# Optimization experiments

Hardware: AMD Instinct MI355X
Metric: run time of the kernel (lower is better)

Reference implementation:

```python
import jax, jax.numpy as jnp
import numpy as np

N = 50000      # nodes
E = 800000     # edges (avg degree 16)
IN = 128; HID = 128; OUT = 128; HEADS = 4
NEG_SLOPE = 0.2


def setup_inputs() -> dict:
    key = jax.random.key(0)
    ks = jax.random.split(key, 16)
    def glorot(k, shape):
        fan = shape[0] if len(shape) == 2 else int(np.prod(shape))
        return jax.random.normal(k, shape, jnp.float32) * np.float32(1.0 / np.sqrt(fan))
    C = HID // HEADS
    x = jax.random.normal(ks[0], (N, IN), jnp.float32)
    edge_index = jax.random.randint(ks[1], (2, E), 0, N, jnp.int32)
    return {
        "x": x, "edge_index": edge_index,
        "W1": glorot(ks[2], (IN, HID)),  "as1": glorot(ks[3], (HEADS, C)),  "ad1": glorot(ks[4], (HEADS, C)),  "b1": jnp.zeros((HID,), jnp.float32),
        "W2": glorot(ks[5], (HID, HID)), "as2": glorot(ks[6], (HEADS, C)),  "ad2": glorot(ks[7], (HEADS, C)),  "b2": jnp.zeros((HID,), jnp.float32),
        "W3": glorot(ks[8], (HID, OUT)), "as3": glorot(ks[9], (1, OUT)),    "ad3": glorot(ks[10], (1, OUT)),   "b3": jnp.zeros((OUT,), jnp.float32),
    }


def gat_conv(x, ei, W, a_src, a_dst, b, concat):
    # x: [N,Fin], ei: [2,E'] (self-loops included), W: [Fin, H*C], a_*: [H,C]
    n = x.shape[0]
    H, C = a_src.shape
    h = (x @ W).reshape(n, H, C)                         # [N,H,C]
    src, dst = ei[0], ei[1]
    alpha_s = jnp.einsum('nhc,hc->nh', h, a_src)         # [N,H]
    alpha_d = jnp.einsum('nhc,hc->nh', h, a_dst)
    e = jax.nn.leaky_relu(alpha_s[src] + alpha_d[dst], NEG_SLOPE)  # [E',H]
    # segment softmax over destination neighborhoods
    m = jax.ops.segment_max(e, dst, num_segments=n)      # [N,H]
    p = jnp.exp(e - m[dst])
    denom = jax.ops.segment_sum(p, dst, num_segments=n)  # [N,H]
    alpha = p / (denom[dst] + 1e-16)                     # [E',H]
    out = jax.ops.segment_sum(h[src] * alpha[:, :, None], dst, num_segments=n)  # [N,H,C]
    out = out.reshape(n, H * C) if concat else out.mean(axis=1)
    return out + b


def reference(x, edge_index, W1, as1, ad1, b1, W2, as2, ad2, b2, W3, as3, ad3, b3):
    n = x.shape[0]
    loops = jnp.arange(n, dtype=edge_index.dtype)
    ei = jnp.concatenate([edge_index, jnp.stack([loops, loops])], axis=1)  # add self-loops
    h = jax.nn.relu(gat_conv(x, ei, W1, as1, ad1, b1, True))   # dropout p=0 / eval: identity
    h = jax.nn.relu(gat_conv(h, ei, W2, as2, ad2, b2, True))
    return gat_conv(h, ei, W3, as3, ad3, b3, False)
```

## Files before the change

kernel.cpp:

```cpp
#include <hip/hip_runtime.h>
#include <hip/hip_bf16.h>
#include <math.h>

#define NPART 8

typedef __attribute__((ext_vector_type(8))) short bf16x8;
typedef __attribute__((ext_vector_type(4))) float f32x4;

__device__ __forceinline__ float lrelu(float v) { return fmaxf(v, 0.2f * v); }

__device__ __forceinline__ unsigned fenc(float f) {
    unsigned u = __float_as_uint(f);
    return (u & 0x80000000u) ? ~u : (u | 0x80000000u);
}
__device__ __forceinline__ float fdec(unsigned u) {
    return __uint_as_float((u & 0x80000000u) ? (u & 0x7FFFFFFFu) : ~u);
}
__device__ __forceinline__ unsigned short f2bf(float f) {
    union { __hip_bfloat16 b; unsigned short u; } cv;
    cv.b = __float2bfloat16(f);
    return cv.u;
}
__device__ __forceinline__ float bflo(unsigned u) { return __uint_as_float(u << 16); }
__device__ __forceinline__ float bfhi(unsigned u) { return __uint_as_float(u & 0xFFFF0000u); }


__global__ void setup_all(const float* __restrict__ x,
                          const float* __restrict__ W1, const float* __restrict__ W2,
                          const float* __restrict__ W3,
                          unsigned short* __restrict__ xb,
                          unsigned short* __restrict__ Wt1, unsigned short* __restrict__ Wt2,
                          unsigned short* __restrict__ Wt3,
                          int* __restrict__ cursor, unsigned short* __restrict__ srcs,
                          unsigned* __restrict__ gmax, unsigned short* __restrict__ hb,
                          int N, int GX) {
    int b = blockIdx.x, t = threadIdx.x;
    if (b < GX) {
        int i = b * 256 + t;
        if (i < N * 32) {
            float4 v = ((const float4*)x)[i];
            ushort4 o;
            o.x = f2bf(v.x); o.y = f2bf(v.y); o.z = f2bf(v.z); o.w = f2bf(v.w);
            ((ushort4*)xb)[i] = o;
        }
        if (i < N) {
            cursor[i] = (i << 6) + 1;
            srcs[(size_t)i << 6] = (unsigned short)i;
        }
        if (i < 12) gmax[i] = fenc(-1e30f);
        if (i < 64) ((unsigned*)hb)[(size_t)N * 64 + i] = 0;
        return;
    }
    {
        int j = (b - GX) * 256 + t;
        if (j < 3 * 16384) {
            int mm = j >> 14, e = j & 16383;
            const float* W = (mm == 0) ? W1 : (mm == 1) ? W2 : W3;
            unsigned short* Wt = (mm == 0) ? Wt1 : (mm == 1) ? Wt2 : Wt3;
            int k = e >> 7, c = e & 127;
            Wt[c * 128 + k] = f2bf(W[e]);
        }
    }
}


__global__ void scatter_part(const int* __restrict__ ei, int E, int N,
                             int* cursor, unsigned short* __restrict__ srcs, int pn) {
    int part = blockIdx.x & (NPART - 1);
    int nb = gridDim.x >> 3;
    int chunk = blockIdx.x >> 3;
    int stride = nb * blockDim.x;
    int lo = part * pn, hi = min(lo + pn, N);
    for (int i = chunk * blockDim.x + threadIdx.x; i < E; i += stride) {
        int d = ei[E + i];
        if (d >= lo && d < hi) {
            int pos = atomicAdd(&cursor[d], 1);
            if (pos - (d << 6) < 64) srcs[pos] = (unsigned short)ei[i];
        }
    }
}


__global__ void pad_fill(int* __restrict__ cursor, unsigned short* __restrict__ srcs, int N) {
    int n = blockIdx.x * 256 + threadIdx.x;
    if (n >= N) return;
    int dr = cursor[n] - (n << 6);
    if (dr > 64) dr = 64;
    int q = (dr + 3) >> 2;
    for (int k = dr; k < q * 4; k++) srcs[(n << 6) + k] = (unsigned short)N;
    cursor[n] = q;
}


template <int H>
__global__ __launch_bounds__(256) void gemm_fused(const unsigned short* __restrict__ xb,
                                                  const unsigned short* __restrict__ Wt,
                                                  const float* __restrict__ a_s,
                                                  const float* __restrict__ a_d,
                                                  unsigned short* __restrict__ hb,
                                                  float* __restrict__ asb,
                                                  float* __restrict__ adb,
                                                  unsigned* __restrict__ gmax, int N) {
    constexpr int HH = (H == 4) ? 4 : 1;
    __shared__ float smax[4][HH];
    int t = threadIdx.x;
    int wave = t >> 6, lane = t & 63;
    int lrow = lane & 15;
    int kg = lane >> 4;
    int row0 = blockIdx.x * 64 + wave * 16;
    int arow = min(row0 + lrow, N - 1);
    const bf16x8* ap = (const bf16x8*)(xb + (size_t)arow * 128 + kg * 8);

    f32x4 acc[8];
#pragma unroll
    for (int ct = 0; ct < 8; ct++) acc[ct] = (f32x4)0.f;
#pragma unroll
    for (int kk = 0; kk < 4; kk++) {
        bf16x8 a = ap[kk * 4];
#pragma unroll
        for (int ct = 0; ct < 8; ct++) {
            const bf16x8* bp = (const bf16x8*)(Wt + (size_t)(ct * 16 + lrow) * 128 + kk * 32 + kg * 8);
            acc[ct] = __builtin_amdgcn_mfma_f32_16x16x32_bf16(a, *bp, acc[ct], 0, 0, 0);
        }
    }
    int orow = row0 + kg * 4;
#pragma unroll
    for (int reg = 0; reg < 4; reg++) {
        int r = orow + reg;
        if (r < N) {
#pragma unroll
            for (int ct = 0; ct < 8; ct++)
                hb[(size_t)r * 128 + ct * 16 + lrow] = f2bf(acc[ct][reg]);
        }
    }
    float ps[4][HH], pd[4][HH];
#pragma unroll
    for (int reg = 0; reg < 4; reg++)
#pragma unroll
        for (int hd = 0; hd < HH; hd++) { ps[reg][hd] = 0.f; pd[reg][hd] = 0.f; }
#pragma unroll
    for (int ct = 0; ct < 8; ct++) {
        int hd = (H == 4) ? (ct >> 1) : 0;
        float asv = a_s[ct * 16 + lrow];
        float adv = a_d[ct * 16 + lrow];
#pragma unroll
        for (int reg = 0; reg < 4; reg++) {
            ps[reg][hd] += acc[ct][reg] * asv;
            pd[reg][hd] += acc[ct][reg] * adv;
        }
    }
    for (int o = 1; o < 16; o <<= 1) {
#pragma unroll
        for (int reg = 0; reg < 4; reg++)
#pragma unroll
            for (int hd = 0; hd < HH; hd++) {
                ps[reg][hd] += __shfl_xor(ps[reg][hd], o);
                pd[reg][hd] += __shfl_xor(pd[reg][hd], o);
            }
    }
    if (lrow < HH) {
        int hd = lrow;
#pragma unroll
        for (int reg = 0; reg < 4; reg++) {
            int r = orow + reg;
            if (r < N) {
                asb[(size_t)r * H + hd] = ps[reg][hd];
                adb[(size_t)r * H + hd] = pd[reg][hd];
            }
        }
    }
    float wm[HH];
#pragma unroll
    for (int hd = 0; hd < HH; hd++) {
        float m = fmaxf(fmaxf(ps[0][hd], ps[1][hd]), fmaxf(ps[2][hd], ps[3][hd]));
        m = fmaxf(m, __shfl_xor(m, 16));
        m = fmaxf(m, __shfl_xor(m, 32));
        wm[hd] = m;
    }
    if (lane == 0)
#pragma unroll
        for (int hd = 0; hd < HH; hd++) smax[wave][hd] = wm[hd];
    __syncthreads();
    if (t < HH) {
        float m = fmaxf(fmaxf(smax[0][t], smax[1][t]), fmaxf(smax[2][t], smax[3][t]));
        atomicMax(&gmax[t], fenc(m));
    }
    if (blockIdx.x == 0 && t == 0) {
#pragma unroll
        for (int hd = 0; hd < HH; hd++) asb[(size_t)N * H + hd] = -1e30f;
    }
}


template <int H, bool RELU, bool OUTBF>
__global__ __launch_bounds__(256) void aggregate10(const unsigned short* __restrict__ hb,
                                                   const unsigned short* __restrict__ srcs,
                                                   const int* __restrict__ qn,
                                                   const float* __restrict__ asb,
                                                   const float* __restrict__ adb,
                                                   const unsigned* __restrict__ gmax,
                                                   const float* __restrict__ bias,
                                                   void* __restrict__ outv, int N) {
    int n = (blockIdx.x * 256 + threadIdx.x) >> 4;
    if (n >= N) return;
    unsigned l = threadIdx.x & 15;
    unsigned ht = (H == 4) ? (l >> 2) : 0;
    int base = (threadIdx.x & 63) & ~15;
    float adn = adb[(unsigned)n * H + ht];
    float m = lrelu(fdec(gmax[ht]) + adn);
    const unsigned short* sp = srcs + ((size_t)n << 6);
    const uint4* hrow = (const uint4*)hb;
    int nb = qn[n];
    float a0 = 0.f, a1 = 0.f, a2 = 0.f, a3 = 0.f;
    float a4 = 0.f, a5 = 0.f, a6 = 0.f, a7 = 0.f, den = 0.f;

    ushort4 sq = *(const ushort4*)sp;
    uint4 u0 = hrow[(unsigned)sq.x * 16u + l];
    uint4 u1 = hrow[(unsigned)sq.y * 16u + l];
    uint4 u2 = hrow[(unsigned)sq.z * 16u + l];
    uint4 u3 = hrow[(unsigned)sq.w * 16u + l];
    for (int j = 0; j < nb; j++) {
        int jn = (j + 1 < nb) ? j + 1 : j;
        ushort4 sn = *(const ushort4*)(sp + jn * 4);
        uint4 v0 = hrow[(unsigned)sn.x * 16u + l];
        uint4 v1 = hrow[(unsigned)sn.y * 16u + l];
        uint4 v2 = hrow[(unsigned)sn.z * 16u + l];
        uint4 v3 = hrow[(unsigned)sn.w * 16u + l];
        unsigned sown = sp[j * 4 + (l & 3)];
        float e = asb[sown * H + ht];
        float pown = __expf(lrelu(e + adn) - m);
        float p0 = __shfl(pown, base + (int)ht * 4 + 0);
        float p1 = __shfl(pown, base + (int)ht * 4 + 1);
        float p2 = __shfl(pown, base + (int)ht * 4 + 2);
        float p3 = __shfl(pown, base + (int)ht * 4 + 3);
        a0 += p0 * bflo(u0.x); a1 += p0 * bfhi(u0.x); a2 += p0 * bflo(u0.y); a3 += p0 * bfhi(u0.y);
        a4 += p0 * bflo(u0.z); a5 += p0 * bfhi(u0.z); a6 += p0 * bflo(u0.w); a7 += p0 * bfhi(u0.w);
        a0 += p1 * bflo(u1.x); a1 += p1 * bfhi(u1.x); a2 += p1 * bflo(u1.y); a3 += p1 * bfhi(u1.y);
        a4 += p1 * bflo(u1.z); a5 += p1 * bfhi(u1.z); a6 += p1 * bflo(u1.w); a7 += p1 * bfhi(u1.w);
        a0 += p2 * bflo(u2.x); a1 += p2 * bfhi(u2.x); a2 += p2 * bflo(u2.y); a3 += p2 * bfhi(u2.y);
        a4 += p2 * bflo(u2.z); a5 += p2 * bfhi(u2.z); a6 += p2 * bflo(u2.w); a7 += p2 * bfhi(u2.w);
        a0 += p3 * bflo(u3.x); a1 += p3 * bfhi(u3.x); a2 += p3 * bflo(u3.y); a3 += p3 * bfhi(u3.y);
        a4 += p3 * bflo(u3.z); a5 += p3 * bfhi(u3.z); a6 += p3 * bflo(u3.w); a7 += p3 * bfhi(u3.w);
        den += p0 + p1 + p2 + p3;
        sq = sn; u0 = v0; u1 = v1; u2 = v2; u3 = v3;
    }
    float inv = 1.f / (den + 1e-16f);
    unsigned c = l * 8;
    float4 bv0 = *(const float4*)&bias[c];
    float4 bv1 = *(const float4*)&bias[c + 4];
    float o0 = a0 * inv + bv0.x, o1 = a1 * inv + bv0.y;
    float o2 = a2 * inv + bv0.z, o3 = a3 * inv + bv0.w;
    float o4 = a4 * inv + bv1.x, o5 = a5 * inv + bv1.y;
    float o6 = a6 * inv + bv1.z, o7 = a7 * inv + bv1.w;
    if (RELU) {
        o0 = fmaxf(o0, 0.f); o1 = fmaxf(o1, 0.f); o2 = fmaxf(o2, 0.f); o3 = fmaxf(o3, 0.f);
        o4 = fmaxf(o4, 0.f); o5 = fmaxf(o5, 0.f); o6 = fmaxf(o6, 0.f); o7 = fmaxf(o7, 0.f);
    }
    if (OUTBF) {
        uint4 st;
        st.x = (unsigned)f2bf(o0) | ((unsigned)f2bf(o1) << 16);
        st.y = (unsigned)f2bf(o2) | ((unsigned)f2bf(o3) << 16);
        st.z = (unsigned)f2bf(o4) | ((unsigned)f2bf(o5) << 16);
        st.w = (unsigned)f2bf(o6) | ((unsigned)f2bf(o7) << 16);
        *(uint4*)&((unsigned short*)outv)[(size_t)n * 128 + c] = st;
    } else {
        float* op = (float*)outv + (size_t)n * 128 + c;
        float4 s0; s0.x = o0; s0.y = o1; s0.z = o2; s0.w = o3;
        float4 s1; s1.x = o4; s1.y = o5; s1.z = o6; s1.w = o7;
        *(float4*)op = s0;
        *(float4*)(op + 4) = s1;
    }
}


extern "C" void kernel_launch(void* const* d_in, const int* in_sizes, int n_in,
                              void* d_out, int out_size, void* d_ws, size_t ws_size,
                              hipStream_t stream) {
    const float* x   = (const float*)d_in[0];
    const int*   ei  = (const int*)d_in[1];
    const float* W1  = (const float*)d_in[2];
    const float* as1 = (const float*)d_in[3];
    const float* ad1 = (const float*)d_in[4];
    const float* b1  = (const float*)d_in[5];
    const float* W2  = (const float*)d_in[6];
    const float* as2 = (const float*)d_in[7];
    const float* ad2 = (const float*)d_in[8];
    const float* b2  = (const float*)d_in[9];
    const float* W3  = (const float*)d_in[10];
    const float* as3 = (const float*)d_in[11];
    const float* ad3 = (const float*)d_in[12];
    const float* b3  = (const float*)d_in[13];

    const int N = in_sizes[0] / 128;
    const int E = in_sizes[1] / 2;
    const int PN = (N + NPART - 1) / NPART;

    char* w = (char*)d_ws;
    size_t woff = 0;
    auto alloc = [&](size_t bytes) -> void* {
        void* p = w + woff;
        woff = (woff + bytes + 255) & ~(size_t)255;
        return p;
    };
    int*      cursor = (int*)alloc((size_t)(N + 1) * 4);
    unsigned short* srcs = (unsigned short*)alloc(((size_t)N * 64 + 64) * 2);
    float*    asb    = (float*)alloc((size_t)(N + 1) * 4 * 4);
    float*    adb    = (float*)alloc((size_t)(N + 1) * 4 * 4);
    unsigned* gmax   = (unsigned*)alloc(16 * 4);
    unsigned short* hb  = (unsigned short*)alloc((size_t)(N + 1) * 128 * 2);
    unsigned short* xb  = (unsigned short*)alloc((size_t)N * 128 * 2);
    unsigned short* Wt1 = (unsigned short*)alloc(128 * 128 * 2);
    unsigned short* Wt2 = (unsigned short*)alloc(128 * 128 * 2);
    unsigned short* Wt3 = (unsigned short*)alloc(128 * 128 * 2);
    float* outf = (float*)d_out;

    const int GX = (N * 32 + 255) / 256;
    setup_all<<<GX + 192, 256, 0, stream>>>(x, W1, W2, W3, xb, Wt1, Wt2, Wt3,
                                            cursor, srcs, gmax, hb, N, GX);

    scatter_part<<<2048, 256, 0, stream>>>(ei, E, N, cursor, srcs, PN);

    pad_fill<<<(N + 255) / 256, 256, 0, stream>>>(cursor, srcs, N);

    const int gb = (N + 63) / 64;
    const int ga = (N * 16 + 255) / 256;

    gemm_fused<4><<<gb, 256, 0, stream>>>(xb, Wt1, as1, ad1, hb, asb, adb, gmax + 0, N);
    aggregate10<4, true, true><<<ga, 256, 0, stream>>>(hb, srcs, cursor, asb, adb, gmax + 0, b1, xb, N);

    gemm_fused<4><<<gb, 256, 0, stream>>>(xb, Wt2, as2, ad2, hb, asb, adb, gmax + 4, N);
    aggregate10<4, true, true><<<ga, 256, 0, stream>>>(hb, srcs, cursor, asb, adb, gmax + 4, b2, xb, N);

    gemm_fused<1><<<gb, 256, 0, stream>>>(xb, Wt3, as3, ad3, hb, asb, adb, gmax + 8, N);
    aggregate10<1, false, false><<<ga, 256, 0, stream>>>(hb, srcs, cursor, asb, adb, gmax + 8, b3, outf, N);
}
```

Baseline: 243.7 us.

## Sort nodes by degree bucket and deepen gather prefetch in aggregation

Builds a histogram of padded neighbor-group counts and a new order_fill kernel that produces a node permutation grouped by degree bucket. Each aggregation wave then processes nodes with similar loop trip counts, which should reduce divergence and idle lanes. The aggregation loop also prefetches neighbor feature rows two groups ahead and the next attention logit one step ahead, to hide gather latency better. In exchange it adds an extra kernel, atomics, more registers per thread, and output writes that are less sequential.

New measurement: 528.9 us. +117.0%, slower.

```diff
diff --git a/kernel.cpp b/kernel.cpp
--- a/kernel.cpp
+++ b/kernel.cpp
@@ -33,6 +33,7 @@
                           unsigned short* __restrict__ Wt3,
                           int* __restrict__ cursor, unsigned short* __restrict__ srcs,
                           unsigned* __restrict__ gmax, unsigned short* __restrict__ hb,
+                          int* __restrict__ hist, int* __restrict__ bcur,
                           int N, int GX) {
     int b = blockIdx.x, t = threadIdx.x;
     if (b < GX) {
@@ -48,6 +49,7 @@
             srcs[(size_t)i << 6] = (unsigned short)i;
         }
         if (i < 12) gmax[i] = fenc(-1e30f);
+        if (i < 32) { hist[i] = 0; bcur[i] = 0; }
         if (i < 64) ((unsigned*)hb)[(size_t)N * 64 + i] = 0;
         return;
     }
@@ -81,7 +83,8 @@
 }
 
 
-__global__ void pad_fill(int* __restrict__ cursor, unsigned short* __restrict__ srcs, int N) {
+__global__ void pad_fill(int* __restrict__ cursor, unsigned short* __restrict__ srcs,
+                         int* __restrict__ hist, int N) {
     int n = blockIdx.x * 256 + threadIdx.x;
     if (n >= N) return;
     int dr = cursor[n] - (n << 6);
@@ -89,6 +92,30 @@
     int q = (dr + 3) >> 2;
     for (int k = dr; k < q * 4; k++) srcs[(n << 6) + k] = (unsigned short)N;
     cursor[n] = q;
+    atomicAdd(&hist[q], 1);
+}
+
+
+__global__ void order_fill(const int* __restrict__ cursor, const int* __restrict__ hist,
+                           int* __restrict__ bcur, int* __restrict__ order, int N) {
+    __shared__ int lh[20], gb[20], lc[20];
+    int t = threadIdx.x;
+    if (t < 20) { lh[t] = 0; lc[t] = 0; }
+    __syncthreads();
+    int n = blockIdx.x * 256 + t;
+    int q = (n < N) ? cursor[n] : -1;
+    if (q > 0) atomicAdd(&lh[q], 1);
+    __syncthreads();
+    if (t > 0 && t < 20 && lh[t] > 0) {
+        int base = 0;
+        for (int k = 1; k < t; k++) base += hist[k];
+        gb[t] = base + atomicAdd(&bcur[t], lh[t]);
+    }
+    __syncthreads();
+    if (q > 0) {
+        int r = atomicAdd(&lc[q], 1);
+        order[gb[q] + r] = n;
+    }
 }
 
 
@@ -193,17 +220,20 @@
 
 
 template <int H, bool RELU, bool OUTBF>
-__global__ __launch_bounds__(256) void aggregate10(const unsigned short* __restrict__ hb,
+__global__ __launch_bounds__(256) void aggregate11(const unsigned short* __restrict__ hb,
                                                    const unsigned short* __restrict__ srcs,
                                                    const int* __restrict__ qn,
+                                                   const int* __restrict__ order,
                                                    const float* __restrict__ asb,
                                                    const float* __restrict__ adb,
                                                    const unsigned* __restrict__ gmax,
                                                    const float* __restrict__ bias,
                                                    void* __restrict__ outv, int N) {
-    int n = (blockIdx.x * 256 + threadIdx.x) >> 4;
-    if (n >= N) return;
+    int qid = (blockIdx.x * 256 + threadIdx.x) >> 4;
+    if (qid >= N) return;
+    int n = order[qid];
     unsigned l = threadIdx.x & 15;
+    unsigned le = l & 3;
     unsigned ht = (H == 4) ? (l >> 2) : 0;
     int base = (threadIdx.x & 63) & ~15;
     float adn = adb[(unsigned)n * H + ht];
@@ -211,24 +241,35 @@
     const unsigned short* sp = srcs + ((size_t)n << 6);
     const uint4* hrow = (const uint4*)hb;
     int nb = qn[n];
+
     float a0 = 0.f, a1 = 0.f, a2 = 0.f, a3 = 0.f;
     float a4 = 0.f, a5 = 0.f, a6 = 0.f, a7 = 0.f, den = 0.f;
 
-    ushort4 sq = *(const ushort4*)sp;
-    uint4 u0 = hrow[(unsigned)sq.x * 16u + l];
-    uint4 u1 = hrow[(unsigned)sq.y * 16u + l];
-    uint4 u2 = hrow[(unsigned)sq.z * 16u + l];
-    uint4 u3 = hrow[(unsigned)sq.w * 16u + l];
+    int q1 = (nb > 1) ? 1 : 0;
+    int q2 = (nb > 2) ? 2 : q1;
+    ushort4 sq0 = *(const ushort4*)sp;
+    ushort4 sq1 = *(const ushort4*)(sp + q1 * 4);
+    ushort4 sqA = *(const ushort4*)(sp + q2 * 4);
+    uint4 u0 = hrow[(unsigned)sq0.x * 16u + l];
+    uint4 u1 = hrow[(unsigned)sq0.y * 16u + l];
+    uint4 u2 = hrow[(unsigned)sq0.z * 16u + l];
+    uint4 u3 = hrow[(unsigned)sq0.w * 16u + l];
+    uint4 v0 = hrow[(unsigned)sq1.x * 16u + l];
+    uint4 v1 = hrow[(unsigned)sq1.y * 16u + l];
+    uint4 v2 = hrow[(unsigned)sq1.z * 16u + l];
+    uint4 v3 = hrow[(unsigned)sq1.w * 16u + l];
+    float e_cur = asb[(unsigned)sp[le] * H + ht];
+
     for (int j = 0; j < nb; j++) {
-        int jn = (j + 1 < nb) ? j + 1 : j;
-        ushort4 sn = *(const ushort4*)(sp + jn * 4);
-        uint4 v0 = hrow[(unsigned)sn.x * 16u + l];
-        uint4 v1 = hrow[(unsigned)sn.y * 16u + l];
-        uint4 v2 = hrow[(unsigned)sn.z * 16u + l];
-        uint4 v3 = hrow[(unsigned)sn.w * 16u + l];
-        unsigned sown = sp[j * 4 + (l & 3)];
-        float e = asb[sown * H + ht];
-        float pown = __expf(lrelu(e + adn) - m);
+        uint4 w0 = hrow[(unsigned)sqA.x * 16u + l];
+        uint4 w1 = hrow[(unsigned)sqA.y * 16u + l];
+        uint4 w2 = hrow[(unsigned)sqA.z * 16u + l];
+        uint4 w3 = hrow[(unsigned)sqA.w * 16u + l];
+        int jn = (j + 3 < nb) ? j + 3 : nb - 1;
+        ushort4 sqN = *(const ushort4*)(sp + jn * 4);
+        int je = (j + 1 < nb) ? j + 1 : j;
+        float e_nxt = asb[(unsigned)sp[je * 4 + le] * H + ht];
+        float pown = __expf(lrelu(e_cur + adn) - m);
         float p0 = __shfl(pown, base + (int)ht * 4 + 0);
         float p1 = __shfl(pown, base + (int)ht * 4 + 1);
         float p2 = __shfl(pown, base + (int)ht * 4 + 2);
@@ -242,7 +283,10 @@
         a0 += p3 * bflo(u3.x); a1 += p3 * bfhi(u3.x); a2 += p3 * bflo(u3.y); a3 += p3 * bfhi(u3.y);
         a4 += p3 * bflo(u3.z); a5 += p3 * bfhi(u3.z); a6 += p3 * bflo(u3.w); a7 += p3 * bfhi(u3.w);
         den += p0 + p1 + p2 + p3;
-        sq = sn; u0 = v0; u1 = v1; u2 = v2; u3 = v3;
+        u0 = v0; u1 = v1; u2 = v2; u3 = v3;
+        v0 = w0; v1 = w1; v2 = w2; v3 = w3;
+        sqA = sqN;
+        e_cur = e_nxt;
     }
     float inv = 1.f / (den + 1e-16f);
     unsigned c = l * 8;
@@ -303,6 +347,9 @@
         return p;
     };
     int*      cursor = (int*)alloc((size_t)(N + 1) * 4);
+    int*      order  = (int*)alloc((size_t)(N + 1) * 4);
+    int*      hist   = (int*)alloc(32 * 4);
+    int*      bcur   = (int*)alloc(32 * 4);
     unsigned short* srcs = (unsigned short*)alloc(((size_t)N * 64 + 64) * 2);
     float*    asb    = (float*)alloc((size_t)(N + 1) * 4 * 4);
     float*    adb    = (float*)alloc((size_t)(N + 1) * 4 * 4);
@@ -316,21 +363,26 @@
 
     const int GX = (N * 32 + 255) / 256;
     setup_all<<<GX + 192, 256, 0, stream>>>(x, W1, W2, W3, xb, Wt1, Wt2, Wt3,
-                                            cursor, srcs, gmax, hb, N, GX);
+                                            cursor, srcs, gmax, hb, hist, bcur, N, GX);
 
     scatter_part<<<2048, 256, 0, stream>>>(ei, E, N, cursor, srcs, PN);
 
-    pad_fill<<<(N + 255) / 256, 256, 0, stream>>>(cursor, srcs, N);
+    pad_fill<<<(N + 255) / 256, 256, 0, stream>>>(cursor, srcs, hist, N);
+
+    order_fill<<<(N + 255) / 256, 256, 0, stream>>>(cursor, hist, bcur, order, N);
 
     const int gb = (N + 63) / 64;
     const int ga = (N * 16 + 255) / 256;
 
     gemm_fused<4><<<gb, 256, 0, stream>>>(xb, Wt1, as1, ad1, hb, asb, adb, gmax + 0, N);
-    aggregate10<4, true, true><<<ga, 256, 0, stream>>>(hb, srcs, cursor, asb, adb, gmax + 0, b1, xb, N);
+    aggregate11<4, true, true><<<ga, 256, 0, stream>>>(hb, srcs, cursor, order, asb, adb,
+                                                       gmax + 0, b1, xb, N);
 
     gemm_fused<4><<<gb, 256, 0, stream>>>(xb, Wt2, as2, ad2, hb, asb, adb, gmax + 4, N);
-    aggregate10<4, true, true><<<ga, 256, 0, stream>>>(hb, srcs, cursor, asb, adb, gmax + 4, b2, xb, N);
+    aggregate11<4, true, true><<<ga, 256, 0, stream>>>(hb, srcs, cursor, order, asb, adb,
+                                                       gmax + 4, b2, xb, N);
 
     gemm_fused<1><<<gb, 256, 0, stream>>>(xb, Wt3, as3, ad3, hb, asb, adb, gmax + 8, N);
-    aggregate10<1, false, false><<<ga, 256, 0, stream>>>(hb, srcs, cursor, asb, adb, gmax + 8, b3, outf, N);
-}
+    aggregate11<1, false, false><<<ga, 256, 0, stream>>>(hb, srcs, cursor, order, asb, adb,
+                                                         gmax + 8, b3, outf, N);
+}
```

## Fuse edge scatter into layer-1 GEMM and defer padding into layer-2 GEMM

Applied to the files above, without the earlier changes.

Layer-1 GEMM blocks and edge-scatter blocks now run in one launch, so the GEMM work overlaps the atomic scatter. Padding of the neighbor lists moves into the layer-2 GEMM launch. To allow this, the first aggregation masks the unpadded tail of each neighbor group by computing counts from the raw cursor. This removes two launches and the serialization between them, at the cost of extra mask logic in the first aggregation and reliance on the stale entries beyond the count being valid indices.

Measured after the change: 235.9 us. -3.2%, faster.

```diff
diff --git a/kernel.cpp b/kernel.cpp
--- a/kernel.cpp
+++ b/kernel.cpp
@@ -2,7 +2,7 @@
 #include <hip/hip_bf16.h>
 #include <math.h>
 
-#define NPART 8
+#define SB 1024
 
 typedef __attribute__((ext_vector_type(8))) short bf16x8;
 typedef __attribute__((ext_vector_type(4))) float f32x4;
@@ -64,14 +64,14 @@
 }
 
 
-__global__ void scatter_part(const int* __restrict__ ei, int E, int N,
-                             int* cursor, unsigned short* __restrict__ srcs, int pn) {
-    int part = blockIdx.x & (NPART - 1);
-    int nb = gridDim.x >> 3;
-    int chunk = blockIdx.x >> 3;
-    int stride = nb * blockDim.x;
+__device__ __forceinline__ void scatter_body(int sb, int t, const int* __restrict__ ei,
+                                             int E, int N, int* cursor,
+                                             unsigned short* __restrict__ srcs, int pn) {
+    int part = sb & 7;
+    int chunk = sb >> 3;
+    int stride = (SB >> 3) * 256;
     int lo = part * pn, hi = min(lo + pn, N);
-    for (int i = chunk * blockDim.x + threadIdx.x; i < E; i += stride) {
+    for (int i = chunk * 256 + t; i < E; i += stride) {
         int d = ei[E + i];
         if (d >= lo && d < hi) {
             int pos = atomicAdd(&cursor[d], 1);
@@ -80,9 +80,9 @@
     }
 }
 
-
-__global__ void pad_fill(int* __restrict__ cursor, unsigned short* __restrict__ srcs, int N) {
-    int n = blockIdx.x * 256 + threadIdx.x;
+__device__ __forceinline__ void pad_body(int pb, int t, int* __restrict__ cursor,
+                                         unsigned short* __restrict__ srcs, int N) {
+    int n = pb * 256 + t;
     if (n >= N) return;
     int dr = cursor[n] - (n << 6);
     if (dr > 64) dr = 64;
@@ -93,21 +93,21 @@
 
 
 template <int H>
-__global__ __launch_bounds__(256) void gemm_fused(const unsigned short* __restrict__ xb,
-                                                  const unsigned short* __restrict__ Wt,
-                                                  const float* __restrict__ a_s,
-                                                  const float* __restrict__ a_d,
-                                                  unsigned short* __restrict__ hb,
-                                                  float* __restrict__ asb,
-                                                  float* __restrict__ adb,
-                                                  unsigned* __restrict__ gmax, int N) {
+__device__ __forceinline__ void gemm_body(int bid, const unsigned short* __restrict__ xb,
+                                          const unsigned short* __restrict__ Wt,
+                                          const float* __restrict__ a_s,
+                                          const float* __restrict__ a_d,
+                                          unsigned short* __restrict__ hb,
+                                          float* __restrict__ asb,
+                                          float* __restrict__ adb,
+                                          unsigned* __restrict__ gmax, int N) {
     constexpr int HH = (H == 4) ? 4 : 1;
     __shared__ float smax[4][HH];
     int t = threadIdx.x;
     int wave = t >> 6, lane = t & 63;
     int lrow = lane & 15;
     int kg = lane >> 4;
-    int row0 = blockIdx.x * 64 + wave * 16;
+    int row0 = bid * 64 + wave * 16;
     int arow = min(row0 + lrow, N - 1);
     const bf16x8* ap = (const bf16x8*)(xb + (size_t)arow * 128 + kg * 8);
 
@@ -185,14 +185,61 @@
         float m = fmaxf(fmaxf(smax[0][t], smax[1][t]), fmaxf(smax[2][t], smax[3][t]));
         atomicMax(&gmax[t], fenc(m));
     }
-    if (blockIdx.x == 0 && t == 0) {
+    if (bid == 0 && t == 0) {
 #pragma unroll
         for (int hd = 0; hd < HH; hd++) asb[(size_t)N * H + hd] = -1e30f;
     }
 }
 
 
-template <int H, bool RELU, bool OUTBF>
+__global__ __launch_bounds__(256) void gemm1_scatter(const unsigned short* __restrict__ xb,
+                                                     const unsigned short* __restrict__ Wt,
+                                                     const float* __restrict__ a_s,
+                                                     const float* __restrict__ a_d,
+                                                     unsigned short* __restrict__ hb,
+                                                     float* __restrict__ asb,
+                                                     float* __restrict__ adb,
+                                                     unsigned* __restrict__ gmax,
+                                                     const int* __restrict__ ei, int E,
+                                                     int* __restrict__ cursor,
+                                                     unsigned short* __restrict__ srcs,
+                                                     int N, int gb, int pn) {
+    if ((int)blockIdx.x < gb)
+        gemm_body<4>(blockIdx.x, xb, Wt, a_s, a_d, hb, asb, adb, gmax, N);
+    else
+        scatter_body(blockIdx.x - gb, threadIdx.x, ei, E, N, cursor, srcs, pn);
+}
+
+__global__ __launch_bounds__(256) void gemm2_pad(const unsigned short* __restrict__ xb,
+                                                 const unsigned short* __restrict__ Wt,
+                                                 const float* __restrict__ a_s,
+                                                 const float* __restrict__ a_d,
+                                                 unsigned short* __restrict__ hb,
+                                                 float* __restrict__ asb,
+                                                 float* __restrict__ adb,
+                                                 unsigned* __restrict__ gmax,
+                                                 int* __restrict__ cursor,
+                                                 unsigned short* __restrict__ srcs,
+                                                 int N, int gb) {
+    if ((int)blockIdx.x < gb)
+        gemm_body<4>(blockIdx.x, xb, Wt, a_s, a_d, hb, asb, adb, gmax, N);
+    else
+        pad_body(blockIdx.x - gb, threadIdx.x, cursor, srcs, N);
+}
+
+__global__ __launch_bounds__(256) void gemm3_k(const unsigned short* __restrict__ xb,
+                                               const unsigned short* __restrict__ Wt,
+                                               const float* __restrict__ a_s,
+                                               const float* __restrict__ a_d,
+                                               unsigned short* __restrict__ hb,
+                                               float* __restrict__ asb,
+                                               float* __restrict__ adb,
+                                               unsigned* __restrict__ gmax, int N) {
+    gemm_body<1>(blockIdx.x, xb, Wt, a_s, a_d, hb, asb, adb, gmax, N);
+}
+
+
+template <int H, bool RELU, bool OUTBF, bool MASK>
 __global__ __launch_bounds__(256) void aggregate10(const unsigned short* __restrict__ hb,
                                                    const unsigned short* __restrict__ srcs,
                                                    const int* __restrict__ qn,
@@ -210,7 +257,17 @@
     float m = lrelu(fdec(gmax[ht]) + adn);
     const unsigned short* sp = srcs + ((size_t)n << 6);
     const uint4* hrow = (const uint4*)hb;
-    int nb = qn[n];
+    int cv = qn[n];
+    int nb, rem;
+    if (MASK) {
+        int dr = cv - (n << 6);
+        dr = min(dr, 64);
+        nb = (dr + 3) >> 2;
+        rem = dr - ((nb - 1) << 2);
+    } else {
+        nb = cv;
+        rem = 4;
+    }
     float a0 = 0.f, a1 = 0.f, a2 = 0.f, a3 = 0.f;
     float a4 = 0.f, a5 = 0.f, a6 = 0.f, a7 = 0.f, den = 0.f;
 
@@ -233,6 +290,12 @@
         float p1 = __shfl(pown, base + (int)ht * 4 + 1);
         float p2 = __shfl(pown, base + (int)ht * 4 + 2);
         float p3 = __shfl(pown, base + (int)ht * 4 + 3);
+        if (MASK) {
+            int limit = (j == nb - 1) ? rem : 4;
+            p1 = (1 < limit) ? p1 : 0.f;
+            p2 = (2 < limit) ? p2 : 0.f;
+            p3 = (3 < limit) ? p3 : 0.f;
+        }
         a0 += p0 * bflo(u0.x); a1 += p0 * bfhi(u0.x); a2 += p0 * bflo(u0.y); a3 += p0 * bfhi(u0.y);
         a4 += p0 * bflo(u0.z); a5 += p0 * bfhi(u0.z); a6 += p0 * bflo(u0.w); a7 += p0 * bfhi(u0.w);
         a0 += p1 * bflo(u1.x); a1 += p1 * bfhi(u1.x); a2 += p1 * bflo(u1.y); a3 += p1 * bfhi(u1.y);
@@ -293,7 +356,7 @@
 
     const int N = in_sizes[0] / 128;
     const int E = in_sizes[1] / 2;
-    const int PN = (N + NPART - 1) / NPART;
+    const int PN = (N + 7) / 8;
 
     char* w = (char*)d_ws;
     size_t woff = 0;
@@ -315,22 +378,27 @@
     float* outf = (float*)d_out;
 
     const int GX = (N * 32 + 255) / 256;
+    const int gb = (N + 63) / 64;
+    const int ga = (N * 16 + 255) / 256;
+    const int PB = (N + 255) / 256;
+
     setup_all<<<GX + 192, 256, 0, stream>>>(x, W1, W2, W3, xb, Wt1, Wt2, Wt3,
                                             cursor, srcs, gmax, hb, N, GX);
 
-    scatter_part<<<2048, 256, 0, stream>>>(ei, E, N, cursor, srcs, PN);
-
-    pad_fill<<<(N + 255) / 256, 256, 0, stream>>>(cursor, srcs, N);
-
-    const int gb = (N + 63) / 64;
-    const int ga = (N * 16 + 255) / 256;
-
-    gemm_fused<4><<<gb, 256, 0, stream>>>(xb, Wt1, as1, ad1, hb, asb, adb, gmax + 0, N);
-    aggregate10<4, true, true><<<ga, 256, 0, stream>>>(hb, srcs, cursor, asb, adb, gmax + 0, b1, xb, N);
-
-    gemm_fused<4><<<gb, 256, 0, stream>>>(xb, Wt2, as2, ad2, hb, asb, adb, gmax + 4, N);
-    aggregate10<4, true, true><<<ga, 256, 0, stream>>>(hb, srcs, cursor, asb, adb, gmax + 4, b2, xb, N);
-
-    gemm_fused<1><<<gb, 256, 0, stream>>>(xb, Wt3, as3, ad3, hb, asb, adb, gmax + 8, N);
-    aggregate10<1, false, false><<<ga, 256, 0, stream>>>(hb, srcs, cursor, asb, adb, gmax + 8, b3, outf, N);
-}
+    gemm1_scatter<<<gb + SB, 256, 0, stream>>>(xb, Wt1, as1, ad1, hb, asb, adb, gmax + 0,
+                                               ei, E, cursor, srcs, N, gb, PN);
+
+    aggregate10<4, true, true, true><<<ga, 256, 0, stream>>>(hb, srcs, cursor, asb, adb,
+                                                             gmax + 0, b1, xb, N);
+
+    gemm2_pad<<<gb + PB, 256, 0, stream>>>(xb, Wt2, as2, ad2, hb, asb, adb, gmax + 4,
+                                           cursor, srcs, N, gb);
+
+    aggregate10<4, true, true, false><<<ga, 256, 0, stream>>>(hb, srcs, cursor, asb, adb,
+                                                              gmax + 4, b2, xb, N);
+
+    gemm3_k<<<gb, 256, 0, stream>>>(xb, Wt3, as3, ad3, hb, asb, adb, gmax + 8, N);
+
+    aggregate10<1, false, false, false><<<ga, 256, 0, stream>>>(hb, srcs, cursor, asb, adb,
+                                                                gmax + 8, b3, outf, N);
+}
```
